# Optimization experiments

Hardware: AMD Instinct MI355X
Metric: run time of the kernel (lower is better)

Reference implementation:

```python
import jax, jax.numpy as jnp
import numpy as np

NB_HEAD = 16

def setup_inputs() -> dict:
    key = jax.random.key(0)
    ks = jax.random.split(key, 5)
    B, S, E = 2, 2048, 1024
    sc = 1.0 / np.sqrt(E)
    x = jax.random.normal(ks[0], (B, S, E), dtype=jnp.float32)
    Wq = jax.random.normal(ks[1], (E, E), dtype=jnp.float32) * sc
    Wk = jax.random.normal(ks[2], (E, E), dtype=jnp.float32) * sc
    Wv = jax.random.normal(ks[3], (E, E), dtype=jnp.float32) * sc
    Wo = jax.random.normal(ks[4], (E, E), dtype=jnp.float32) * sc
    z = jnp.zeros((E,), dtype=jnp.float32)
    return {"x": x, "Wq": Wq, "bq": z, "Wk": Wk, "bk": z, "Wv": Wv, "bv": z, "Wo": Wo, "bo": z}

def reference(x, Wq, bq, Wk, bk, Wv, bv, Wo, bo):
    B, S, E = x.shape
    H = NB_HEAD
    D = E // H
    # projections -> [B, S, H, D]
    q = (x @ Wq + bq).reshape(B, S, H, D)
    k = (x @ Wk + bk).reshape(B, S, H, D)
    v = (x @ Wv + bv).reshape(B, S, H, D)
    # NOTE: original scales by sqrt(embedding_size), not sqrt(head_dim)
    scores = jnp.einsum('bqhd,bkhd->bhqk', q, k) / jnp.sqrt(jnp.float32(E))
    causal = jnp.tril(jnp.ones((S, S), dtype=bool))  # mask=True path
    scores = jnp.where(causal[None, None], scores, -jnp.inf)
    p = jax.nn.softmax(scores, axis=-1)
    attn = jnp.einsum('bhqk,bkhd->bqhd', p, v).reshape(B, S, E)
    return attn @ Wo + bo
```

## Files before the change

### kernel.cpp

```cpp
#include <hip/hip_runtime.h>
#include <hip/hip_bf16.h>

#define S_LEN 2048
#define EMB   1024
#define NHEAD 16
#define HDIM  64
#define NBATCH 2
#define M_ROWS (NBATCH * S_LEN)

typedef __attribute__((ext_vector_type(8))) __bf16 bf16x8;
typedef __attribute__((ext_vector_type(8))) short short8;
typedef __attribute__((ext_vector_type(4))) short short4_t;
typedef __attribute__((ext_vector_type(4))) float floatx4;

__device__ inline bf16x8 load_frag(const short* p) {
    short8 v = *(const short8*)p;
    return __builtin_bit_cast(bf16x8, v);
}
__device__ inline floatx4 mfma16(bf16x8 a, bf16x8 b, floatx4 c) {
    return __builtin_amdgcn_mfma_f32_16x16x32_bf16(a, b, c, 0, 0, 0);
}
__device__ inline short f2bf_bits(float f) {
    return __builtin_bit_cast(short, __float2bfloat16(f));
}

#if defined(__has_builtin)
#if __has_builtin(__builtin_amdgcn_global_load_lds)
#define HAVE_ASYNC_LDS 1
#endif
#endif

#ifdef HAVE_ASYNC_LDS
typedef __attribute__((address_space(1))) const void glb_void;
typedef __attribute__((address_space(3))) void lds_void;
__device__ __forceinline__ void load16_to_lds(const void* g, void* l) {
    __builtin_amdgcn_global_load_lds((glb_void*)g, (lds_void*)l, 16, 0, 0);
}
#endif

__global__ __launch_bounds__(256) void prep_kernel(
        const float* __restrict__ x, short* __restrict__ xb,
        const float* __restrict__ w0, const float* __restrict__ w1,
        const float* __restrict__ w2, const float* __restrict__ w3,
        short* __restrict__ o0, short* __restrict__ o1,
        short* __restrict__ o2, short* __restrict__ o3) {
    const int t = threadIdx.x;
    if (blockIdx.x < 2048) {
        int idx = (blockIdx.x * 256 + t) * 8;
        float4 a = *(const float4*)&x[idx];
        float4 b = *(const float4*)&x[idx + 4];
        short8 o;
        o[0] = f2bf_bits(a.x); o[1] = f2bf_bits(a.y);
        o[2] = f2bf_bits(a.z); o[3] = f2bf_bits(a.w);
        o[4] = f2bf_bits(b.x); o[5] = f2bf_bits(b.y);
        o[6] = f2bf_bits(b.z); o[7] = f2bf_bits(b.w);
        *(short8*)&xb[idx] = o;
    } else {
        __shared__ float tile[32][33];
        int tb = blockIdx.x - 2048;
        int z = tb >> 10, rem = tb & 1023;
        int bx = rem & 31, by = rem >> 5;
        const float* in; short* out;
        switch (z) {
            case 0: in = w0; out = o0; break;
            case 1: in = w1; out = o1; break;
            case 2: in = w2; out = o2; break;
            default: in = w3; out = o3; break;
        }
        int tx = t & 31, ty = t >> 5;
        int c = bx * 32 + tx;
        int r0 = by * 32;
#pragma unroll
        for (int i = 0; i < 4; i++) {
            int r = r0 + ty + i * 8;
            tile[ty + i * 8][tx] = in[(size_t)r * EMB + c];
        }
        __syncthreads();
        int rr = r0 + tx;
        int cc0 = bx * 32;
#pragma unroll
        for (int i = 0; i < 4; i++) {
            int cc = cc0 + ty + i * 8;
            out[(size_t)cc * EMB + rr] = f2bf_bits(tile[tx][ty + i * 8]);
        }
    }
}

__global__ __launch_bounds__(256, 2) void qkv_fused(
        const short* __restrict__ x,
        const short* __restrict__ WqT, const short* __restrict__ WkT,
        const short* __restrict__ WvT,
        const float* __restrict__ pbq, const float* __restrict__ pbk,
        const float* __restrict__ pbv,
        short* __restrict__ Q, short* __restrict__ K, short* __restrict__ Vt) {
    __shared__ short lds_a[128 * 64];
    __shared__ short lds_b[3][64 * 64];

    const int t = threadIdx.x;
    const int wave = t >> 6, lane = t & 63;
    const int wm = wave >> 1, wn = wave & 1;
    const int l15 = lane & 15, quad = lane >> 4;
    const int rowA0 = blockIdx.x * 128;
    const int colB0 = blockIdx.y * 64;

    const short* Bts[3] = {WqT, WkT, WvT};

    floatx4 acc[3][4][2] = {};

    for (int k0 = 0; k0 < EMB; k0 += 64) {
#pragma unroll
        for (int i = 0; i < 4; i++) {
            int idx = i * 256 + t;
            int row = idx >> 3;
            int cg = ((idx & 7) ^ (row & 7)) * 8;
            const short* ga = &x[(size_t)(rowA0 + row) * EMB + k0 + cg];
#ifdef HAVE_ASYNC_LDS
            load16_to_lds(ga, &lds_a[(i * 256 + wave * 64) * 8]);
#else
            *(short8*)&lds_a[idx * 8] = *(const short8*)ga;
#endif
        }
#pragma unroll
        for (int m = 0; m < 3; m++)
#pragma unroll
            for (int i = 0; i < 2; i++) {
                int idx = i * 256 + t;
                int row = idx >> 3;
                int cg = ((idx & 7) ^ (row & 7)) * 8;
                const short* gb = &Bts[m][(size_t)(colB0 + row) * EMB + k0 + cg];
#ifdef HAVE_ASYNC_LDS
                load16_to_lds(gb, &lds_b[m][(i * 256 + wave * 64) * 8]);
#else
                *(short8*)&lds_b[m][idx * 8] = *(const short8*)gb;
#endif
            }
        __syncthreads();
#pragma unroll
        for (int kk = 0; kk < 2; kk++) {
            bf16x8 af[4];
#pragma unroll
            for (int i = 0; i < 4; i++)
                af[i] = load_frag(&lds_a[(wm * 64 + i * 16 + l15) * 64 +
                                         (((kk * 4 + quad) ^ (l15 & 7)) * 8)]);
#pragma unroll
            for (int m = 0; m < 3; m++)
#pragma unroll
                for (int j = 0; j < 2; j++) {
                    bf16x8 bfr = load_frag(
                        &lds_b[m][(wn * 32 + j * 16 + l15) * 64 +
                                  (((kk * 4 + quad) ^ (l15 & 7)) * 8)]);
#pragma unroll
                    for (int i = 0; i < 4; i++)
                        acc[m][i][j] = mfma16(af[i], bfr, acc[m][i][j]);
                }
        }
        __syncthreads();
    }

#pragma unroll
    for (int i = 0; i < 4; i++)
#pragma unroll
        for (int j = 0; j < 2; j++) {
            int col = colB0 + wn * 32 + j * 16 + l15;
            int h = col >> 6, d = col & 63;
            int row0 = rowA0 + wm * 64 + i * 16 + quad * 4;
            int b = row0 >> 11, s0 = row0 & 2047;
            float bvq = pbq[col], bvk = pbk[col], bvv = pbv[col];
#pragma unroll
            for (int r = 0; r < 4; r++)
                Q[((size_t)((b * NHEAD + h) * S_LEN + s0 + r)) * HDIM + d] =
                    f2bf_bits(acc[0][i][j][r] + bvq);
#pragma unroll
            for (int r = 0; r < 4; r++)
                K[((size_t)((b * NHEAD + h) * S_LEN + s0 + r)) * HDIM + d] =
                    f2bf_bits(acc[1][i][j][r] + bvk);
            short4_t pack;
#pragma unroll
            for (int r = 0; r < 4; r++)
                pack[r] = f2bf_bits(acc[2][i][j][r] + bvv);
            *(short4_t*)&Vt[((size_t)((b * NHEAD + h) * HDIM + d)) * S_LEN + s0] = pack;
        }
}

__global__ __launch_bounds__(256) void out_gemm(
        const short* __restrict__ A, const short* __restrict__ Bt,
        const float* __restrict__ bias, float* __restrict__ Cout) {
    __shared__ short lds_a[128 * 64];
    __shared__ short lds_b[64 * 64];

    const int t = threadIdx.x;
    const int wave = t >> 6, lane = t & 63;
    const int wm = wave >> 1, wn = wave & 1;
    const int l15 = lane & 15, quad = lane >> 4;
    const int rowA0 = blockIdx.x * 128;
    const int rowB0 = blockIdx.y * 64;

    floatx4 acc[4][2] = {};

    for (int k0 = 0; k0 < EMB; k0 += 64) {
#pragma unroll
        for (int i = 0; i < 4; i++) {
            int idx = i * 256 + t;
            int row = idx >> 3;
            int cg = ((idx & 7) ^ (row & 7)) * 8;
            const short* ga = &A[(size_t)(rowA0 + row) * EMB + k0 + cg];
#ifdef HAVE_ASYNC_LDS
            load16_to_lds(ga, &lds_a[(i * 256 + wave * 64) * 8]);
#else
            *(short8*)&lds_a[idx * 8] = *(const short8*)ga;
#endif
        }
#pragma unroll
        for (int i = 0; i < 2; i++) {
            int idx = i * 256 + t;
            int row = idx >> 3;
            int cg = ((idx & 7) ^ (row & 7)) * 8;
            const short* gb = &Bt[(size_t)(rowB0 + row) * EMB + k0 + cg];
#ifdef HAVE_ASYNC_LDS
            load16_to_lds(gb, &lds_b[(i * 256 + wave * 64) * 8]);
#else
            *(short8*)&lds_b[idx * 8] = *(const short8*)gb;
#endif
        }
        __syncthreads();
#pragma unroll
        for (int kk = 0; kk < 2; kk++) {
            bf16x8 af[4], bfr[2];
#pragma unroll
            for (int i = 0; i < 4; i++)
                af[i] = load_frag(&lds_a[(wm * 64 + i * 16 + l15) * 64 +
                                         (((kk * 4 + quad) ^ (l15 & 7)) * 8)]);
#pragma unroll
            for (int j = 0; j < 2; j++)
                bfr[j] = load_frag(&lds_b[(wn * 32 + j * 16 + l15) * 64 +
                                          (((kk * 4 + quad) ^ (l15 & 7)) * 8)]);
#pragma unroll
            for (int i = 0; i < 4; i++)
#pragma unroll
                for (int j = 0; j < 2; j++)
                    acc[i][j] = mfma16(af[i], bfr[j], acc[i][j]);
        }
        __syncthreads();
    }

#pragma unroll
    for (int i = 0; i < 4; i++)
#pragma unroll
        for (int j = 0; j < 2; j++) {
            int col = rowB0 + wn * 32 + j * 16 + l15;
            float bv = bias[col];
            int row0 = rowA0 + wm * 64 + i * 16 + quad * 4;
#pragma unroll
            for (int r = 0; r < 4; r++)
                Cout[(size_t)(row0 + r) * EMB + col] = acc[i][j][r] + bv;
        }
}

__global__ __launch_bounds__(256) void attn_kernel(
        const short* __restrict__ Q, const short* __restrict__ K,
        const short* __restrict__ Vt, short* __restrict__ O) {
    constexpr int LDPP = 136;
    __shared__ short lds_k[128 * 64];
    __shared__ short lds_v[64 * 128];
    __shared__ short lds_p[4][16 * LDPP];

    const int t = threadIdx.x;
    const int wave = t >> 6, lane = t & 63;
    const int l15 = lane & 15, quad = lane >> 4;
    const int bh = blockIdx.x;
    const int slot = blockIdx.y;
    const short* Qh = Q + (size_t)bh * S_LEN * HDIM;
    const short* Kh = K + (size_t)bh * S_LEN * HDIM;
    const short* Vh = Vt + (size_t)bh * HDIM * S_LEN;
    const int b = bh >> 4, h = bh & 15;

    const float C1 = 0.03125f * 1.44269504088896f;
    const float M  = 12.0f;

    bf16x8 ones;
    {
        short8 o1v;
        short one = f2bf_bits(1.0f);
#pragma unroll
        for (int i = 0; i < 8; i++) o1v[i] = one;
        ones = __builtin_bit_cast(bf16x8, o1v);
    }

#pragma unroll 1
    for (int phase = 0; phase < 2; phase++) {
        const int qt = phase == 0 ? (31 - slot) : slot;
        const int q0 = qt * 64;
        const int nch = (qt + 2) >> 1;

        const int qrowA = q0 + wave * 16 + l15;
        bf16x8 qf0 = load_frag(&Qh[(size_t)qrowA * HDIM + quad * 8]);
        bf16x8 qf1 = load_frag(&Qh[(size_t)qrowA * HDIM + 32 + quad * 8]);

        floatx4 accO[4] = {};
        floatx4 accL = {};

#pragma unroll 1
        for (int cd = 0; cd < nch; cd++) {
            const int kv0 = cd * 128;
#pragma unroll
            for (int i = 0; i < 4; i++) {
                int idx = i * 256 + t;
                int krow = idx >> 3, kcl = idx & 7;
                int kcg = kcl ^ (krow & 7);
                int vrow = idx >> 4, vcl = idx & 15;
                int vcg = vcl ^ (vrow & 15);
                const short* gk = &Kh[(size_t)(kv0 + krow) * HDIM + kcg * 8];
                const short* gv = &Vh[(size_t)vrow * S_LEN + kv0 + vcg * 8];
#ifdef HAVE_ASYNC_LDS
                int base = (i * 256 + wave * 64) * 8;
                load16_to_lds(gk, &lds_k[base]);
                load16_to_lds(gv, &lds_v[base]);
#else
                *(short8*)&lds_k[idx * 8] = *(const short8*)gk;
                *(short8*)&lds_v[idx * 8] = *(const short8*)gv;
#endif
            }
            __syncthreads();

            floatx4 sacc[8];
#pragma unroll
            for (int c = 0; c < 8; c++) {
                int krow = c * 16 + l15;
                bf16x8 kf0 = load_frag(&lds_k[krow * 64 + (quad ^ (l15 & 7)) * 8]);
                bf16x8 kf1 = load_frag(&lds_k[krow * 64 + ((4 + quad) ^ (l15 & 7)) * 8]);
                floatx4 z = {};
                z = mfma16(qf0, kf0, z);
                sacc[c] = mfma16(qf1, kf1, z);
            }

            if (kv0 + 128 > q0) {
#pragma unroll
                for (int c = 0; c < 8; c++)
#pragma unroll
                    for (int r = 0; r < 4; r++) {
                        int qrow = q0 + wave * 16 + quad * 4 + r;
                        int kcol = kv0 + c * 16 + l15;
                        float p = __builtin_amdgcn_exp2f(
                            __builtin_fmaf(sacc[c][r], C1, -M));
                        p = (kcol > qrow) ? 0.f : p;
                        lds_p[wave][(quad * 4 + r) * LDPP + c * 16 + l15] =
                            f2bf_bits(p);
                    }
            } else {
#pragma unroll
                for (int c = 0; c < 8; c++)
#pragma unroll
                    for (int r = 0; r < 4; r++) {
                        float p = __builtin_amdgcn_exp2f(
                            __builtin_fmaf(sacc[c][r], C1, -M));
                        lds_p[wave][(quad * 4 + r) * LDPP + c * 16 + l15] =
                            f2bf_bits(p);
                    }
            }

#pragma unroll
            for (int ks = 0; ks < 4; ks++) {
                bf16x8 pf = load_frag(&lds_p[wave][l15 * LDPP + ks * 32 + quad * 8]);
                accL = mfma16(pf, ones, accL);
#pragma unroll
                for (int dt = 0; dt < 4; dt++) {
                    int vrow = dt * 16 + l15;
                    bf16x8 vf = load_frag(
                        &lds_v[vrow * 128 + ((ks * 4 + quad) ^ l15) * 8]);
                    accO[dt] = mfma16(pf, vf, accO[dt]);
                }
            }
            __syncthreads();
        }

#pragma unroll
        for (int r = 0; r < 4; r++) {
            float inv = 1.0f / accL[r];
            int q = q0 + wave * 16 + quad * 4 + r;
#pragma unroll
            for (int dt = 0; dt < 4; dt++) {
                int d = dt * 16 + l15;
                O[((size_t)(b * S_LEN + q) * NHEAD + h) * HDIM + d] =
                    f2bf_bits(accO[dt][r] * inv);
            }
        }
    }
}

extern "C" void kernel_launch(void* const* d_in, const int* in_sizes, int n_in,
                              void* d_out, int out_size, void* d_ws, size_t ws_size,
                              hipStream_t stream) {
    const float* x  = (const float*)d_in[0];
    const float* Wq = (const float*)d_in[1];
    const float* bq = (const float*)d_in[2];
    const float* Wk = (const float*)d_in[3];
    const float* bk = (const float*)d_in[4];
    const float* Wv = (const float*)d_in[5];
    const float* bv = (const float*)d_in[6];
    const float* Wo = (const float*)d_in[7];
    const float* bo = (const float*)d_in[8];

    short* ws = (short*)d_ws;
    const size_t WSZ = (size_t)EMB * EMB;
    const size_t TSZ = (size_t)M_ROWS * EMB;
    short* xb  = ws;
    short* WqT = xb + TSZ;
    short* WkT = WqT + WSZ;
    short* WvT = WkT + WSZ;
    short* WoT = WvT + WSZ;
    short* Qb  = WoT + WSZ;
    short* Kb  = Qb + TSZ;
    short* Vtb = Kb + TSZ;
    short* Ab  = Vtb + TSZ;

    prep_kernel<<<dim3(2048 + 4096), 256, 0, stream>>>(
        x, xb, Wq, Wk, Wv, Wo, WqT, WkT, WvT, WoT);

    qkv_fused<<<dim3(M_ROWS / 128, EMB / 64), 256, 0, stream>>>(
        xb, WqT, WkT, WvT, bq, bk, bv, Qb, Kb, Vtb);

    attn_kernel<<<dim3(NBATCH * NHEAD, 16), 256, 0, stream>>>(Qb, Kb, Vtb, Ab);

    out_gemm<<<dim3(M_ROWS / 128, EMB / 64), 256, 0, stream>>>(
        Ab, WoT, bo, (float*)d_out);
}
```

Baseline: 168.7 us.

## Process both causal query tiles concurrently, sharing each K/V chunk load

The attention kernel no longer runs its two query tiles (long and short) one after the other. Waves are split so two handle each tile, and each wave covers 32 query rows with two sub-tiles. One K/V chunk loaded into LDS now serves both tiles, and each K/V fragment read from LDS is reused across two MFMA row blocks. This halves K/V global traffic and the number of sync rounds for the short tile. The cost is idle waves: the short-tile waves sit through barriers while the long tile finishes its extra chunks, and register and LDS use grow.

```diff
diff --git a/kernel.cpp b/kernel.cpp
--- a/kernel.cpp
+++ b/kernel.cpp
@@ -262,7 +262,7 @@
     constexpr int LDPP = 136;
     __shared__ short lds_k[128 * 64];
     __shared__ short lds_v[64 * 128];
-    __shared__ short lds_p[4][16 * LDPP];
+    __shared__ short lds_p[4][32 * LDPP];
 
     const int t = threadIdx.x;
     const int wave = t >> 6, lane = t & 63;
@@ -277,6 +277,13 @@
     const float C1 = 0.03125f * 1.44269504088896f;
     const float M  = 12.0f;
 
+    const int tile = wave >> 1, wsub = wave & 1;
+    const int qt = tile == 0 ? (31 - slot) : slot;
+    const int q0 = qt * 64;
+    const int qbase = q0 + wsub * 32;
+    const int nch_this = (qt + 2) >> 1;
+    const int nch_total = (33 - slot) >> 1;
+
     bf16x8 ones;
     {
         short8 o1v;
@@ -286,105 +293,118 @@
         ones = __builtin_bit_cast(bf16x8, o1v);
     }
 
+    bf16x8 qf[2][2];
+#pragma unroll
+    for (int st = 0; st < 2; st++) {
+        int qrow = qbase + st * 16 + l15;
+        qf[st][0] = load_frag(&Qh[(size_t)qrow * HDIM + quad * 8]);
+        qf[st][1] = load_frag(&Qh[(size_t)qrow * HDIM + 32 + quad * 8]);
+    }
+
+    floatx4 accO[2][4] = {};
+    floatx4 accL[2] = {};
+
 #pragma unroll 1
-    for (int phase = 0; phase < 2; phase++) {
-        const int qt = phase == 0 ? (31 - slot) : slot;
-        const int q0 = qt * 64;
-        const int nch = (qt + 2) >> 1;
-
-        const int qrowA = q0 + wave * 16 + l15;
-        bf16x8 qf0 = load_frag(&Qh[(size_t)qrowA * HDIM + quad * 8]);
-        bf16x8 qf1 = load_frag(&Qh[(size_t)qrowA * HDIM + 32 + quad * 8]);
-
-        floatx4 accO[4] = {};
-        floatx4 accL = {};
-
-#pragma unroll 1
-        for (int cd = 0; cd < nch; cd++) {
-            const int kv0 = cd * 128;
-#pragma unroll
-            for (int i = 0; i < 4; i++) {
-                int idx = i * 256 + t;
-                int krow = idx >> 3, kcl = idx & 7;
-                int kcg = kcl ^ (krow & 7);
-                int vrow = idx >> 4, vcl = idx & 15;
-                int vcg = vcl ^ (vrow & 15);
-                const short* gk = &Kh[(size_t)(kv0 + krow) * HDIM + kcg * 8];
-                const short* gv = &Vh[(size_t)vrow * S_LEN + kv0 + vcg * 8];
-#ifdef HAVE_ASYNC_LDS
-                int base = (i * 256 + wave * 64) * 8;
-                load16_to_lds(gk, &lds_k[base]);
-                load16_to_lds(gv, &lds_v[base]);
+    for (int cd = 0; cd < nch_total; cd++) {
+        const int kv0 = cd * 128;
+#pragma unroll
+        for (int i = 0; i < 4; i++) {
+            int idx = i * 256 + t;
+            int krow = idx >> 3, kcl = idx & 7;
+            int kcg = kcl ^ (krow & 7);
+            int vrow = idx >> 4, vcl = idx & 15;
+            int vcg = vcl ^ (vrow & 15);
+            const short* gk = &Kh[(size_t)(kv0 + krow) * HDIM + kcg * 8];
+            const short* gv = &Vh[(size_t)vrow * S_LEN + kv0 + vcg * 8];
+#ifdef HAVE_ASYNC_LDS
+            int base = (i * 256 + wave * 64) * 8;
+            load16_to_lds(gk, &lds_k[base]);
+            load16_to_lds(gv, &lds_v[base]);
 #else
-                *(short8*)&lds_k[idx * 8] = *(const short8*)gk;
-                *(short8*)&lds_v[idx * 8] = *(const short8*)gv;
-#endif
+            *(short8*)&lds_k[idx * 8] = *(const short8*)gk;
+            *(short8*)&lds_v[idx * 8] = *(const short8*)gv;
+#endif
+        }
+        __syncthreads();
+
+        if (cd < nch_this) {
+            if (kv0 + 128 > qbase) {
+#pragma unroll
+                for (int c = 0; c < 8; c++) {
+                    int krow = c * 16 + l15;
+                    bf16x8 kf0 = load_frag(&lds_k[krow * 64 + (quad ^ (l15 & 7)) * 8]);
+                    bf16x8 kf1 = load_frag(&lds_k[krow * 64 + ((4 + quad) ^ (l15 & 7)) * 8]);
+#pragma unroll
+                    for (int st = 0; st < 2; st++) {
+                        floatx4 z = {};
+                        z = mfma16(qf[st][0], kf0, z);
+                        floatx4 s = mfma16(qf[st][1], kf1, z);
+#pragma unroll
+                        for (int r = 0; r < 4; r++) {
+                            int qrow = qbase + st * 16 + quad * 4 + r;
+                            int kcol = kv0 + c * 16 + l15;
+                            float p = __builtin_amdgcn_exp2f(
+                                __builtin_fmaf(s[r], C1, -M));
+                            p = (kcol > qrow) ? 0.f : p;
+                            lds_p[wave][(st * 16 + quad * 4 + r) * LDPP +
+                                        c * 16 + l15] = f2bf_bits(p);
+                        }
+                    }
+                }
+            } else {
+#pragma unroll
+                for (int c = 0; c < 8; c++) {
+                    int krow = c * 16 + l15;
+                    bf16x8 kf0 = load_frag(&lds_k[krow * 64 + (quad ^ (l15 & 7)) * 8]);
+                    bf16x8 kf1 = load_frag(&lds_k[krow * 64 + ((4 + quad) ^ (l15 & 7)) * 8]);
+#pragma unroll
+                    for (int st = 0; st < 2; st++) {
+                        floatx4 z = {};
+                        z = mfma16(qf[st][0], kf0, z);
+                        floatx4 s = mfma16(qf[st][1], kf1, z);
+#pragma unroll
+                        for (int r = 0; r < 4; r++) {
+                            float p = __builtin_amdgcn_exp2f(
+                                __builtin_fmaf(s[r], C1, -M));
+                            lds_p[wave][(st * 16 + quad * 4 + r) * LDPP +
+                                        c * 16 + l15] = f2bf_bits(p);
+                        }
+                    }
+                }
             }
-            __syncthreads();
-
-            floatx4 sacc[8];
-#pragma unroll
-            for (int c = 0; c < 8; c++) {
-                int krow = c * 16 + l15;
-                bf16x8 kf0 = load_frag(&lds_k[krow * 64 + (quad ^ (l15 & 7)) * 8]);
-                bf16x8 kf1 = load_frag(&lds_k[krow * 64 + ((4 + quad) ^ (l15 & 7)) * 8]);
-                floatx4 z = {};
-                z = mfma16(qf0, kf0, z);
-                sacc[c] = mfma16(qf1, kf1, z);
-            }
-
-            if (kv0 + 128 > q0) {
-#pragma unroll
-                for (int c = 0; c < 8; c++)
-#pragma unroll
-                    for (int r = 0; r < 4; r++) {
-                        int qrow = q0 + wave * 16 + quad * 4 + r;
-                        int kcol = kv0 + c * 16 + l15;
-                        float p = __builtin_amdgcn_exp2f(
-                            __builtin_fmaf(sacc[c][r], C1, -M));
-                        p = (kcol > qrow) ? 0.f : p;
-                        lds_p[wave][(quad * 4 + r) * LDPP + c * 16 + l15] =
-                            f2bf_bits(p);
-                    }
-            } else {
-#pragma unroll
-                for (int c = 0; c < 8; c++)
-#pragma unroll
-                    for (int r = 0; r < 4; r++) {
-                        float p = __builtin_amdgcn_exp2f(
-                            __builtin_fmaf(sacc[c][r], C1, -M));
-                        lds_p[wave][(quad * 4 + r) * LDPP + c * 16 + l15] =
-                            f2bf_bits(p);
-                    }
-            }
 
 #pragma unroll
             for (int ks = 0; ks < 4; ks++) {
-                bf16x8 pf = load_frag(&lds_p[wave][l15 * LDPP + ks * 32 + quad * 8]);
-                accL = mfma16(pf, ones, accL);
+                bf16x8 pf0 = load_frag(&lds_p[wave][l15 * LDPP + ks * 32 + quad * 8]);
+                bf16x8 pf1 = load_frag(&lds_p[wave][(16 + l15) * LDPP + ks * 32 + quad * 8]);
+                accL[0] = mfma16(pf0, ones, accL[0]);
+                accL[1] = mfma16(pf1, ones, accL[1]);
 #pragma unroll
                 for (int dt = 0; dt < 4; dt++) {
                     int vrow = dt * 16 + l15;
                     bf16x8 vf = load_frag(
                         &lds_v[vrow * 128 + ((ks * 4 + quad) ^ l15) * 8]);
-                    accO[dt] = mfma16(pf, vf, accO[dt]);
+                    accO[0][dt] = mfma16(pf0, vf, accO[0][dt]);
+                    accO[1][dt] = mfma16(pf1, vf, accO[1][dt]);
                 }
             }
-            __syncthreads();
-        }
-
+        }
+        __syncthreads();
+    }
+
+#pragma unroll
+    for (int st = 0; st < 2; st++)
 #pragma unroll
         for (int r = 0; r < 4; r++) {
-            float inv = 1.0f / accL[r];
-            int q = q0 + wave * 16 + quad * 4 + r;
+            float inv = 1.0f / accL[st][r];
+            int q = qbase + st * 16 + quad * 4 + r;
 #pragma unroll
             for (int dt = 0; dt < 4; dt++) {
                 int d = dt * 16 + l15;
                 O[((size_t)(b * S_LEN + q) * NHEAD + h) * HDIM + d] =
-                    f2bf_bits(accO[dt][r] * inv);
+                    f2bf_bits(accO[st][dt][r] * inv);
             }
         }
-    }
 }
 
 extern "C" void kernel_launch(void* const* d_in, const int* in_sizes, int n_in,
```

After: 178.0 us. 5.5% more time.
